# Optimization experiments

Measured on AMD Instinct MI355X. Metric: run time of the kernel, lower is better.

The kernel has to match this reference:

```python
import math
import jax, jax.numpy as jnp
import numpy as np

B, D, N, KP1 = 64, 128, 500000, 4096  # batch, input_size, output_size, K+1
MOMENTUM = 0.5


def setup_inputs() -> dict:
    key = jax.random.key(0)
    k0, k1, k2, k3, k4, k5 = jax.random.split(key, 6)
    stdv = 1.0 / math.sqrt(D / 3)
    image = jax.random.normal(k0, (B, D), jnp.float32)
    gene = jax.random.normal(k1, (B, D), jnp.float32)
    index = jax.random.randint(k2, (B,), 0, N, dtype=jnp.int32)
    idx = jax.random.randint(k3, (B, KP1), 0, N, dtype=jnp.int32)
    idx = idx.at[:, 0].set(index)  # positive sample in slot 0
    memory_image = jax.random.uniform(k4, (N, D), jnp.float32) * (2 * stdv) - stdv
    memory_gene = jax.random.uniform(k5, (N, D), jnp.float32) * (2 * stdv) - stdv
    return {"image": image, "gene": gene, "memory_image": memory_image,
            "memory_gene": memory_gene, "index": index, "idx": idx}


def _momentum_update(mem, x, index):
    # gather positive rows, momentum blend, L2 normalize, scatter back
    pos = mem[index] * MOMENTUM + x * (1.0 - MOMENTUM)          # [B, D]
    pos = pos / jnp.sqrt(jnp.sum(pos * pos, axis=1, keepdims=True))
    return mem.at[index].set(pos)


def reference(image, gene, memory_image, memory_gene, index, idx):
    # gathered bank rows are detached in the original (weights .detach())
    w_gene = jax.lax.stop_gradient(memory_gene[idx])    # [B, K+1, D]
    w_image = jax.lax.stop_gradient(memory_image[idx])  # [B, K+1, D]
    # bmm([B,K+1,D], [B,D,1]) -> scores [B, K+1]; use_softmax=False branch:
    # stabilized softmax over the K+1 candidates (no temperature division)
    out_image = jax.nn.softmax(jnp.einsum('bkd,bd->bk', w_gene, image), axis=1)
    out_gene = jax.nn.softmax(jnp.einsum('bkd,bd->bk', w_image, gene), axis=1)
    # no_grad momentum scatter-update of the banks
    new_mem_image = _momentum_update(memory_image, jax.lax.stop_gradient(image), index)
    new_mem_gene = _momentum_update(memory_gene, jax.lax.stop_gradient(gene), index)
    return out_image, out_gene, new_mem_image, new_mem_gene
```

## Files before the change

kernel.cpp:

```cpp
#include <hip/hip_runtime.h>
#include <math.h>

constexpr int Bb   = 64;
constexpr int Dd   = 128;
constexpr int KP1  = 4096;
constexpr long NMEM = 500000L * 128;
constexpr int BK   = Bb * KP1;

typedef float f4 __attribute__((ext_vector_type(4)));


__device__ __forceinline__ float dot8(float4 a, float4 b, float4 x0, float4 x1) {
    return a.x*x0.x + a.y*x0.y + a.z*x0.z + a.w*x0.w
         + b.x*x1.x + b.y*x1.y + b.z*x1.z + b.w*x1.w;
}

__global__ __launch_bounds__(512) void fused_scores_copy(
    const float* __restrict__ image, const float* __restrict__ gene,
    const float* __restrict__ mem_image, const float* __restrict__ mem_gene,
    const int* __restrict__ idx, float* __restrict__ out, int nCopyBlocks)
{
    const int tid = threadIdx.x;

    if (blockIdx.x >= 128) {
        const long half = NMEM / 4;
        const int  cb   = blockIdx.x - 128;
        const int  bank = cb & 1;
        const f4* src = bank ? (const f4*)mem_gene : (const f4*)mem_image;
        f4* dst = (f4*)(out + 2 * BK) + (long)bank * half;
        const long stride = (long)(nCopyBlocks >> 1) * 512;
        long i = (long)(cb >> 1) * 512 + tid;
        for (; i + 3 * stride < half; i += 4 * stride) {
            f4 v0 = src[i];
            f4 v1 = src[i + stride];
            f4 v2 = src[i + 2 * stride];
            f4 v3 = src[i + 3 * stride];
            __builtin_nontemporal_store(v0, dst + i);
            __builtin_nontemporal_store(v1, dst + i + stride);
            __builtin_nontemporal_store(v2, dst + i + 2 * stride);
            __builtin_nontemporal_store(v3, dst + i + 3 * stride);
        }
        for (; i < half; i += stride)
            __builtin_nontemporal_store(src[i], dst + i);
        return;
    }

    const int b     = blockIdx.x >> 1;
    const int which = blockIdx.x & 1;
    const float* w = which ? mem_image : mem_gene;
    const float* x = which ? gene : image;
    float* o = out + (long)which * BK + (long)b * KP1;

    __shared__ int   sidx[KP1];
    __shared__ float sv[KP1];
    __shared__ float red[8];

    {
        const int4* s4 = (const int4*)(idx + (long)b * KP1);
        int4* d4 = (int4*)sidx;
        d4[tid]       = s4[tid];
        d4[tid + 512] = s4[tid + 512];
    }

    const int lg  = tid & 15;
    const int grp = tid >> 4;

    float4 x0 = *(const float4*)(x + b * Dd + lg * 8);
    float4 x1 = *(const float4*)(x + b * Dd + lg * 8 + 4);
    __syncthreads();

    for (int j = 0; j < 128; j += 4) {
        const int k0 = grp + (j + 0) * 32;
        const int k1 = grp + (j + 1) * 32;
        const int k2 = grp + (j + 2) * 32;
        const int k3 = grp + (j + 3) * 32;
        const float4* r0 = (const float4*)(w + (long)sidx[k0] * Dd + lg * 8);
        const float4* r1 = (const float4*)(w + (long)sidx[k1] * Dd + lg * 8);
        const float4* r2 = (const float4*)(w + (long)sidx[k2] * Dd + lg * 8);
        const float4* r3 = (const float4*)(w + (long)sidx[k3] * Dd + lg * 8);
        float4 a0 = r0[0], b0 = r0[1];
        float4 a1 = r1[0], b1 = r1[1];
        float4 a2 = r2[0], b2 = r2[1];
        float4 a3 = r3[0], b3 = r3[1];
        float d0 = dot8(a0, b0, x0, x1);
        float d1 = dot8(a1, b1, x0, x1);
        float d2 = dot8(a2, b2, x0, x1);
        float d3 = dot8(a3, b3, x0, x1);
        d0 += __shfl_xor(d0, 1); d1 += __shfl_xor(d1, 1);
        d2 += __shfl_xor(d2, 1); d3 += __shfl_xor(d3, 1);
        d0 += __shfl_xor(d0, 2); d1 += __shfl_xor(d1, 2);
        d2 += __shfl_xor(d2, 2); d3 += __shfl_xor(d3, 2);
        d0 += __shfl_xor(d0, 4); d1 += __shfl_xor(d1, 4);
        d2 += __shfl_xor(d2, 4); d3 += __shfl_xor(d3, 4);
        d0 += __shfl_xor(d0, 8); d1 += __shfl_xor(d1, 8);
        d2 += __shfl_xor(d2, 8); d3 += __shfl_xor(d3, 8);
        if (lg == 0) {
            sv[k0] = d0; sv[k1] = d1; sv[k2] = d2; sv[k3] = d3;
        }
    }
    __syncthreads();

    float m = -INFINITY;
    for (int k = tid; k < KP1; k += 512) m = fmaxf(m, sv[k]);
    #pragma unroll
    for (int off = 1; off < 64; off <<= 1) m = fmaxf(m, __shfl_xor(m, off));
    if ((tid & 63) == 0) red[tid >> 6] = m;
    __syncthreads();
    if (tid < 64) {
        float tv = (tid < 8) ? red[tid] : -INFINITY;
        #pragma unroll
        for (int off = 1; off < 8; off <<= 1) tv = fmaxf(tv, __shfl_xor(tv, off));
        if (tid == 0) red[0] = tv;
    }
    __syncthreads();
    m = red[0];
    __syncthreads();

    float sum = 0.f;
    for (int k = tid; k < KP1; k += 512) {
        float e = expf(sv[k] - m);
        sv[k] = e;
        sum += e;
    }
    #pragma unroll
    for (int off = 1; off < 64; off <<= 1) sum += __shfl_xor(sum, off);
    if ((tid & 63) == 0) red[tid >> 6] = sum;
    __syncthreads();
    if (tid < 64) {
        float tv = (tid < 8) ? red[tid] : 0.f;
        #pragma unroll
        for (int off = 1; off < 8; off <<= 1) tv += __shfl_xor(tv, off);
        if (tid == 0) red[0] = tv;
    }
    __syncthreads();
    const float inv = 1.0f / red[0];
    for (int k = tid; k < KP1; k += 512) o[k] = sv[k] * inv;
}

__global__ __launch_bounds__(128) void momentum_update(
    const float* __restrict__ image, const float* __restrict__ gene,
    const float* __restrict__ mem_image, const float* __restrict__ mem_gene,
    const int* __restrict__ index, float* __restrict__ out)
{
    const int b     = blockIdx.x;
    const int which = blockIdx.y;
    const float* mem = which ? mem_gene : mem_image;
    const float* x   = which ? gene : image;
    float* o = out + 2 * BK + (long)which * NMEM;

    const long row = index[b];
    const int d = threadIdx.x;

    float p = mem[row * Dd + d] * 0.5f + x[(long)b * Dd + d] * 0.5f;
    float ss = p * p;
    #pragma unroll
    for (int off = 1; off < 64; off <<= 1) ss += __shfl_xor(ss, off);
    __shared__ float r2[2];
    if ((d & 63) == 0) r2[d >> 6] = ss;
    __syncthreads();
    const float inv = 1.0f / sqrtf(r2[0] + r2[1]);
    o[row * Dd + d] = p * inv;
}

extern "C" void kernel_launch(void* const* d_in, const int* in_sizes, int n_in,
                              void* d_out, int out_size, void* d_ws, size_t ws_size,
                              hipStream_t stream) {
    const float* image     = (const float*)d_in[0];
    const float* gene      = (const float*)d_in[1];
    const float* mem_image = (const float*)d_in[2];
    const float* mem_gene  = (const float*)d_in[3];
    const int*   index     = (const int*)d_in[4];
    const int*   idx       = (const int*)d_in[5];
    float* out = (float*)d_out;

    const int nCopy = 1920;
    fused_scores_copy<<<dim3(128 + nCopy), 512, 0, stream>>>(
        image, gene, mem_image, mem_gene, idx, out, nCopy);
    momentum_update<<<dim3(64, 2), 128, 0, stream>>>(
        image, gene, mem_image, mem_gene, index, out);
}
```

Baseline: 214.2 us.

## Split softmax rows across four blocks with a rescaling epilogue

Each score row of 4096 candidates is now split across four blocks of 1024. Each block writes unnormalized exponentials and a per-segment (max, sum) pair to workspace. A new epilogue kernel merges the four partials, rescales the output in place, and also runs the momentum update. This raises score-block parallelism from 128 to 512 blocks so the gather work spreads over more CUs, at the cost of an extra read/write pass over the score outputs. The copy loop unroll is also raised from 4 to 8.

```diff
diff --git a/kernel.cpp b/kernel.cpp
--- a/kernel.cpp
+++ b/kernel.cpp
@@ -7,6 +7,10 @@
 constexpr long NMEM = 500000L * 128;
 constexpr int BK   = Bb * KP1;
 
+constexpr int SPLIT = 4;
+constexpr int CSEG  = KP1 / SPLIT;
+constexpr int NSCORE = Bb * 2 * SPLIT;
+
 typedef float f4 __attribute__((ext_vector_type(4)));
 
 
@@ -18,48 +22,57 @@
 __global__ __launch_bounds__(512) void fused_scores_copy(
     const float* __restrict__ image, const float* __restrict__ gene,
     const float* __restrict__ mem_image, const float* __restrict__ mem_gene,
-    const int* __restrict__ idx, float* __restrict__ out, int nCopyBlocks)
+    const int* __restrict__ idx, float* __restrict__ out,
+    float2* __restrict__ ws, int nCopyBlocks)
 {
     const int tid = threadIdx.x;
 
-    if (blockIdx.x >= 128) {
+    if (blockIdx.x >= NSCORE) {
         const long half = NMEM / 4;
-        const int  cb   = blockIdx.x - 128;
+        const int  cb   = blockIdx.x - NSCORE;
         const int  bank = cb & 1;
         const f4* src = bank ? (const f4*)mem_gene : (const f4*)mem_image;
         f4* dst = (f4*)(out + 2 * BK) + (long)bank * half;
         const long stride = (long)(nCopyBlocks >> 1) * 512;
         long i = (long)(cb >> 1) * 512 + tid;
-        for (; i + 3 * stride < half; i += 4 * stride) {
+        for (; i + 7 * stride < half; i += 8 * stride) {
             f4 v0 = src[i];
             f4 v1 = src[i + stride];
             f4 v2 = src[i + 2 * stride];
             f4 v3 = src[i + 3 * stride];
+            f4 v4 = src[i + 4 * stride];
+            f4 v5 = src[i + 5 * stride];
+            f4 v6 = src[i + 6 * stride];
+            f4 v7 = src[i + 7 * stride];
             __builtin_nontemporal_store(v0, dst + i);
             __builtin_nontemporal_store(v1, dst + i + stride);
             __builtin_nontemporal_store(v2, dst + i + 2 * stride);
             __builtin_nontemporal_store(v3, dst + i + 3 * stride);
+            __builtin_nontemporal_store(v4, dst + i + 4 * stride);
+            __builtin_nontemporal_store(v5, dst + i + 5 * stride);
+            __builtin_nontemporal_store(v6, dst + i + 6 * stride);
+            __builtin_nontemporal_store(v7, dst + i + 7 * stride);
         }
         for (; i < half; i += stride)
             __builtin_nontemporal_store(src[i], dst + i);
         return;
     }
 
-    const int b     = blockIdx.x >> 1;
-    const int which = blockIdx.x & 1;
+    const int sb    = blockIdx.x;
+    const int seg   = sb & (SPLIT - 1);
+    const int which = (sb >> 2) & 1;
+    const int b     = sb >> 3;
     const float* w = which ? mem_image : mem_gene;
     const float* x = which ? gene : image;
-    float* o = out + (long)which * BK + (long)b * KP1;
-
-    __shared__ int   sidx[KP1];
-    __shared__ float sv[KP1];
+    float* o = out + (long)which * BK + (long)b * KP1 + seg * CSEG;
+
+    __shared__ int   sidx[CSEG];
+    __shared__ float sv[CSEG];
     __shared__ float red[8];
 
-    {
-        const int4* s4 = (const int4*)(idx + (long)b * KP1);
-        int4* d4 = (int4*)sidx;
-        d4[tid]       = s4[tid];
-        d4[tid + 512] = s4[tid + 512];
+    if (tid < 256) {
+        const int4* s4 = (const int4*)(idx + (long)b * KP1 + seg * CSEG);
+        ((int4*)sidx)[tid] = s4[tid];
     }
 
     const int lg  = tid & 15;
@@ -69,7 +82,7 @@
     float4 x1 = *(const float4*)(x + b * Dd + lg * 8 + 4);
     __syncthreads();
 
-    for (int j = 0; j < 128; j += 4) {
+    for (int j = 0; j < 32; j += 4) {
         const int k0 = grp + (j + 0) * 32;
         const int k1 = grp + (j + 1) * 32;
         const int k2 = grp + (j + 2) * 32;
@@ -100,8 +113,7 @@
     }
     __syncthreads();
 
-    float m = -INFINITY;
-    for (int k = tid; k < KP1; k += 512) m = fmaxf(m, sv[k]);
+    float m = fmaxf(sv[tid], sv[tid + 512]);
     #pragma unroll
     for (int off = 1; off < 64; off <<= 1) m = fmaxf(m, __shfl_xor(m, off));
     if ((tid & 63) == 0) red[tid >> 6] = m;
@@ -116,12 +128,11 @@
     m = red[0];
     __syncthreads();
 
-    float sum = 0.f;
-    for (int k = tid; k < KP1; k += 512) {
-        float e = expf(sv[k] - m);
-        sv[k] = e;
-        sum += e;
-    }
+    float e0 = expf(sv[tid] - m);
+    float e1 = expf(sv[tid + 512] - m);
+    o[tid]       = e0;
+    o[tid + 512] = e1;
+    float sum = e0 + e1;
     #pragma unroll
     for (int off = 1; off < 64; off <<= 1) sum += __shfl_xor(sum, off);
     if ((tid & 63) == 0) red[tid >> 6] = sum;
@@ -130,35 +141,56 @@
         float tv = (tid < 8) ? red[tid] : 0.f;
         #pragma unroll
         for (int off = 1; off < 8; off <<= 1) tv += __shfl_xor(tv, off);
-        if (tid == 0) red[0] = tv;
-    }
-    __syncthreads();
-    const float inv = 1.0f / red[0];
-    for (int k = tid; k < KP1; k += 512) o[k] = sv[k] * inv;
-}
-
-__global__ __launch_bounds__(128) void momentum_update(
+        if (tid == 0) ws[((which * Bb + b) << 2) | seg] = make_float2(m, tv);
+    }
+}
+
+__global__ __launch_bounds__(512) void epilogue(
     const float* __restrict__ image, const float* __restrict__ gene,
     const float* __restrict__ mem_image, const float* __restrict__ mem_gene,
-    const int* __restrict__ index, float* __restrict__ out)
+    const int* __restrict__ index, const float2* __restrict__ ws,
+    float* __restrict__ out)
 {
-    const int b     = blockIdx.x;
-    const int which = blockIdx.y;
+    const int tid = threadIdx.x;
+
+    if (blockIdx.x < 128) {
+        const int which = blockIdx.x & 1;
+        const int b     = blockIdx.x >> 1;
+        const float2* p = ws + ((which * Bb + b) << 2);
+        float2 p0 = p[0], p1 = p[1], p2 = p[2], p3 = p[3];
+        float M = fmaxf(fmaxf(p0.x, p1.x), fmaxf(p2.x, p3.x));
+        float s0 = expf(p0.x - M), s1 = expf(p1.x - M);
+        float s2 = expf(p2.x - M), s3 = expf(p3.x - M);
+        float denom = p0.y * s0 + p1.y * s1 + p2.y * s2 + p3.y * s3;
+        const float inv = 1.0f / denom;
+        float scale[SPLIT] = { s0 * inv, s1 * inv, s2 * inv, s3 * inv };
+        float* o = out + (long)which * BK + (long)b * KP1;
+        #pragma unroll
+        for (int r = 0; r < 8; ++r) {
+            int k = tid + r * 512;
+            o[k] *= scale[k >> 10];
+        }
+        return;
+    }
+
+    const int task  = ((blockIdx.x - 128) << 2) | (tid >> 7);
+    const int sub   = tid >> 7;
+    const int d     = tid & 127;
+    const int which = task >> 6;
+    const int b     = task & 63;
     const float* mem = which ? mem_gene : mem_image;
     const float* x   = which ? gene : image;
     float* o = out + 2 * BK + (long)which * NMEM;
 
     const long row = index[b];
-    const int d = threadIdx.x;
-
     float p = mem[row * Dd + d] * 0.5f + x[(long)b * Dd + d] * 0.5f;
     float ss = p * p;
     #pragma unroll
     for (int off = 1; off < 64; off <<= 1) ss += __shfl_xor(ss, off);
-    __shared__ float r2[2];
-    if ((d & 63) == 0) r2[d >> 6] = ss;
-    __syncthreads();
-    const float inv = 1.0f / sqrtf(r2[0] + r2[1]);
+    __shared__ float r2[8];
+    if ((tid & 63) == 0) r2[tid >> 6] = ss;
+    __syncthreads();
+    const float inv = 1.0f / sqrtf(r2[2 * sub] + r2[2 * sub + 1]);
     o[row * Dd + d] = p * inv;
 }
 
@@ -172,10 +204,11 @@
     const int*   index     = (const int*)d_in[4];
     const int*   idx       = (const int*)d_in[5];
     float* out = (float*)d_out;
+    float2* ws = (float2*)d_ws;
 
     const int nCopy = 1920;
-    fused_scores_copy<<<dim3(128 + nCopy), 512, 0, stream>>>(
-        image, gene, mem_image, mem_gene, idx, out, nCopy);
-    momentum_update<<<dim3(64, 2), 128, 0, stream>>>(
-        image, gene, mem_image, mem_gene, index, out);
-}
+    fused_scores_copy<<<dim3(NSCORE + nCopy), 512, 0, stream>>>(
+        image, gene, mem_image, mem_gene, idx, out, ws, nCopy);
+    epilogue<<<dim3(160), 512, 0, stream>>>(
+        image, gene, mem_image, mem_gene, index, ws, out);
+}
```

Measured after the change: 224.7 us. 4.9% more time.

## Use atomic work-stealing chunk queue for bank copy shared with score blocks

Applied to the files above, without the earlier changes.

Replaces the static grid-strided copy split with a dynamic queue: every block, including the 128 score/softmax blocks once they finish, grabs chunks of 8192 float4 via an atomic counter and copies them with 16 loads in flight. This aims to balance the bandwidth-bound copy across all CUs and let score blocks help once done, removing tail imbalance. It adds a counter-reset kernel launch, per-chunk atomics and barriers, and a launch-bounds occupancy hint. Softmax loops are also fully unrolled.

```diff
diff --git a/kernel.cpp b/kernel.cpp
--- a/kernel.cpp
+++ b/kernel.cpp
@@ -7,6 +7,14 @@
 constexpr long NMEM = 500000L * 128;
 constexpr int BK   = Bb * KP1;
 
+constexpr long HALF_F4    = NMEM / 4;
+constexpr int  CHUNK_F4   = 8192;
+constexpr int  FULL_PER_B = 1953;
+constexpr long TAIL_BASE  = (long)FULL_PER_B * CHUNK_F4;
+constexpr int  TAIL_F4    = (int)(HALF_F4 - TAIL_BASE);
+constexpr int  CHUNKS_PER_BANK = FULL_PER_B + 1;
+constexpr int  NCHUNK     = 2 * CHUNKS_PER_BANK;
+
 typedef float f4 __attribute__((ext_vector_type(4)));
 
 
@@ -15,126 +23,150 @@
          + b.x*x1.x + b.y*x1.y + b.z*x1.z + b.w*x1.w;
 }
 
-__global__ __launch_bounds__(512) void fused_scores_copy(
+__global__ __launch_bounds__(64) void zero_ctr(unsigned* ctr) {
+    if (threadIdx.x == 0) *ctr = 0u;
+}
+
+__global__ __launch_bounds__(512, 2) void fused_scores_copy(
     const float* __restrict__ image, const float* __restrict__ gene,
     const float* __restrict__ mem_image, const float* __restrict__ mem_gene,
-    const int* __restrict__ idx, float* __restrict__ out, int nCopyBlocks)
+    const int* __restrict__ idx, float* __restrict__ out, unsigned* __restrict__ ctr)
 {
     const int tid = threadIdx.x;
 
-    if (blockIdx.x >= 128) {
-        const long half = NMEM / 4;
-        const int  cb   = blockIdx.x - 128;
-        const int  bank = cb & 1;
-        const f4* src = bank ? (const f4*)mem_gene : (const f4*)mem_image;
-        f4* dst = (f4*)(out + 2 * BK) + (long)bank * half;
-        const long stride = (long)(nCopyBlocks >> 1) * 512;
-        long i = (long)(cb >> 1) * 512 + tid;
-        for (; i + 3 * stride < half; i += 4 * stride) {
-            f4 v0 = src[i];
-            f4 v1 = src[i + stride];
-            f4 v2 = src[i + 2 * stride];
-            f4 v3 = src[i + 3 * stride];
-            __builtin_nontemporal_store(v0, dst + i);
-            __builtin_nontemporal_store(v1, dst + i + stride);
-            __builtin_nontemporal_store(v2, dst + i + 2 * stride);
-            __builtin_nontemporal_store(v3, dst + i + 3 * stride);
-        }
-        for (; i < half; i += stride)
-            __builtin_nontemporal_store(src[i], dst + i);
-        return;
+    if (blockIdx.x < 128) {
+        const int b     = blockIdx.x >> 1;
+        const int which = blockIdx.x & 1;
+        const float* w = which ? mem_image : mem_gene;
+        const float* x = which ? gene : image;
+        float* o = out + (long)which * BK + (long)b * KP1;
+
+        __shared__ int   sidx[KP1];
+        __shared__ float sv[KP1];
+        __shared__ float red[8];
+
+        {
+            const int4* s4 = (const int4*)(idx + (long)b * KP1);
+            int4* d4 = (int4*)sidx;
+            d4[tid]       = s4[tid];
+            d4[tid + 512] = s4[tid + 512];
+        }
+
+        const int lg  = tid & 15;
+        const int grp = tid >> 4;
+
+        float4 x0 = *(const float4*)(x + b * Dd + lg * 8);
+        float4 x1 = *(const float4*)(x + b * Dd + lg * 8 + 4);
+        __syncthreads();
+
+        for (int j = 0; j < 128; j += 4) {
+            const int k0 = grp + (j + 0) * 32;
+            const int k1 = grp + (j + 1) * 32;
+            const int k2 = grp + (j + 2) * 32;
+            const int k3 = grp + (j + 3) * 32;
+            const float4* r0 = (const float4*)(w + (long)sidx[k0] * Dd + lg * 8);
+            const float4* r1 = (const float4*)(w + (long)sidx[k1] * Dd + lg * 8);
+            const float4* r2 = (const float4*)(w + (long)sidx[k2] * Dd + lg * 8);
+            const float4* r3 = (const float4*)(w + (long)sidx[k3] * Dd + lg * 8);
+            float4 a0 = r0[0], b0 = r0[1];
+            float4 a1 = r1[0], b1 = r1[1];
+            float4 a2 = r2[0], b2 = r2[1];
+            float4 a3 = r3[0], b3 = r3[1];
+            float d0 = dot8(a0, b0, x0, x1);
+            float d1 = dot8(a1, b1, x0, x1);
+            float d2 = dot8(a2, b2, x0, x1);
+            float d3 = dot8(a3, b3, x0, x1);
+            d0 += __shfl_xor(d0, 1); d1 += __shfl_xor(d1, 1);
+            d2 += __shfl_xor(d2, 1); d3 += __shfl_xor(d3, 1);
+            d0 += __shfl_xor(d0, 2); d1 += __shfl_xor(d1, 2);
+            d2 += __shfl_xor(d2, 2); d3 += __shfl_xor(d3, 2);
+            d0 += __shfl_xor(d0, 4); d1 += __shfl_xor(d1, 4);
+            d2 += __shfl_xor(d2, 4); d3 += __shfl_xor(d3, 4);
+            d0 += __shfl_xor(d0, 8); d1 += __shfl_xor(d1, 8);
+            d2 += __shfl_xor(d2, 8); d3 += __shfl_xor(d3, 8);
+            if (lg == 0) {
+                sv[k0] = d0; sv[k1] = d1; sv[k2] = d2; sv[k3] = d3;
+            }
+        }
+        __syncthreads();
+
+        float m = fmaxf(sv[tid], sv[tid + 512]);
+        m = fmaxf(m, fmaxf(sv[tid + 1024], sv[tid + 1536]));
+        m = fmaxf(m, fmaxf(sv[tid + 2048], sv[tid + 2560]));
+        m = fmaxf(m, fmaxf(sv[tid + 3072], sv[tid + 3584]));
+        #pragma unroll
+        for (int off = 1; off < 64; off <<= 1) m = fmaxf(m, __shfl_xor(m, off));
+        if ((tid & 63) == 0) red[tid >> 6] = m;
+        __syncthreads();
+        if (tid < 64) {
+            float tv = (tid < 8) ? red[tid] : -INFINITY;
+            #pragma unroll
+            for (int off = 1; off < 8; off <<= 1) tv = fmaxf(tv, __shfl_xor(tv, off));
+            if (tid == 0) red[0] = tv;
+        }
+        __syncthreads();
+        m = red[0];
+        __syncthreads();
+
+        float sum = 0.f;
+        #pragma unroll
+        for (int r = 0; r < 8; ++r) {
+            int k = tid + r * 512;
+            float e = expf(sv[k] - m);
+            sv[k] = e;
+            sum += e;
+        }
+        #pragma unroll
+        for (int off = 1; off < 64; off <<= 1) sum += __shfl_xor(sum, off);
+        if ((tid & 63) == 0) red[tid >> 6] = sum;
+        __syncthreads();
+        if (tid < 64) {
+            float tv = (tid < 8) ? red[tid] : 0.f;
+            #pragma unroll
+            for (int off = 1; off < 8; off <<= 1) tv += __shfl_xor(tv, off);
+            if (tid == 0) red[0] = tv;
+        }
+        __syncthreads();
+        const float inv = 1.0f / red[0];
+        #pragma unroll
+        for (int r = 0; r < 8; ++r) {
+            int k = tid + r * 512;
+            o[k] = sv[k] * inv;
+        }
     }
 
-    const int b     = blockIdx.x >> 1;
-    const int which = blockIdx.x & 1;
-    const float* w = which ? mem_image : mem_gene;
-    const float* x = which ? gene : image;
-    float* o = out + (long)which * BK + (long)b * KP1;
-
-    __shared__ int   sidx[KP1];
-    __shared__ float sv[KP1];
-    __shared__ float red[8];
-
-    {
-        const int4* s4 = (const int4*)(idx + (long)b * KP1);
-        int4* d4 = (int4*)sidx;
-        d4[tid]       = s4[tid];
-        d4[tid + 512] = s4[tid + 512];
+    const f4* srcI = (const f4*)mem_image;
+    const f4* srcG = (const f4*)mem_gene;
+    f4* dst = (f4*)(out + 2 * BK);
+
+    __shared__ unsigned sc;
+    for (;;) {
+        if (tid == 0) sc = atomicAdd(ctr, 1u);
+        __syncthreads();
+        const unsigned c = sc;
+        __syncthreads();
+        if (c >= NCHUNK) break;
+
+        const int  bank  = (c < CHUNKS_PER_BANK) ? 0 : 1;
+        const int  local = bank ? (int)(c - CHUNKS_PER_BANK) : (int)c;
+        const f4*  sbank = bank ? srcG : srcI;
+        const long dbank = (long)bank * HALF_F4;
+
+        if (local < FULL_PER_B) {
+            const long base = (long)local * CHUNK_F4;
+            f4 v[16];
+            #pragma unroll
+            for (int k = 0; k < 16; ++k) v[k] = sbank[base + k * 512 + tid];
+            #pragma unroll
+            for (int k = 0; k < 16; ++k)
+                __builtin_nontemporal_store(v[k], dst + dbank + base + k * 512 + tid);
+        } else {
+            f4 v0 = sbank[TAIL_BASE + tid];
+            f4 v1 = sbank[TAIL_BASE + 512 + tid];
+            __builtin_nontemporal_store(v0, dst + dbank + TAIL_BASE + tid);
+            __builtin_nontemporal_store(v1, dst + dbank + TAIL_BASE + 512 + tid);
+        }
     }
-
-    const int lg  = tid & 15;
-    const int grp = tid >> 4;
-
-    float4 x0 = *(const float4*)(x + b * Dd + lg * 8);
-    float4 x1 = *(const float4*)(x + b * Dd + lg * 8 + 4);
-    __syncthreads();
-
-    for (int j = 0; j < 128; j += 4) {
-        const int k0 = grp + (j + 0) * 32;
-        const int k1 = grp + (j + 1) * 32;
-        const int k2 = grp + (j + 2) * 32;
-        const int k3 = grp + (j + 3) * 32;
-        const float4* r0 = (const float4*)(w + (long)sidx[k0] * Dd + lg * 8);
-        const float4* r1 = (const float4*)(w + (long)sidx[k1] * Dd + lg * 8);
-        const float4* r2 = (const float4*)(w + (long)sidx[k2] * Dd + lg * 8);
-        const float4* r3 = (const float4*)(w + (long)sidx[k3] * Dd + lg * 8);
-        float4 a0 = r0[0], b0 = r0[1];
-        float4 a1 = r1[0], b1 = r1[1];
-        float4 a2 = r2[0], b2 = r2[1];
-        float4 a3 = r3[0], b3 = r3[1];
-        float d0 = dot8(a0, b0, x0, x1);
-        float d1 = dot8(a1, b1, x0, x1);
-        float d2 = dot8(a2, b2, x0, x1);
-        float d3 = dot8(a3, b3, x0, x1);
-        d0 += __shfl_xor(d0, 1); d1 += __shfl_xor(d1, 1);
-        d2 += __shfl_xor(d2, 1); d3 += __shfl_xor(d3, 1);
-        d0 += __shfl_xor(d0, 2); d1 += __shfl_xor(d1, 2);
-        d2 += __shfl_xor(d2, 2); d3 += __shfl_xor(d3, 2);
-        d0 += __shfl_xor(d0, 4); d1 += __shfl_xor(d1, 4);
-        d2 += __shfl_xor(d2, 4); d3 += __shfl_xor(d3, 4);
-        d0 += __shfl_xor(d0, 8); d1 += __shfl_xor(d1, 8);
-        d2 += __shfl_xor(d2, 8); d3 += __shfl_xor(d3, 8);
-        if (lg == 0) {
-            sv[k0] = d0; sv[k1] = d1; sv[k2] = d2; sv[k3] = d3;
-        }
-    }
-    __syncthreads();
-
-    float m = -INFINITY;
-    for (int k = tid; k < KP1; k += 512) m = fmaxf(m, sv[k]);
-    #pragma unroll
-    for (int off = 1; off < 64; off <<= 1) m = fmaxf(m, __shfl_xor(m, off));
-    if ((tid & 63) == 0) red[tid >> 6] = m;
-    __syncthreads();
-    if (tid < 64) {
-        float tv = (tid < 8) ? red[tid] : -INFINITY;
-        #pragma unroll
-        for (int off = 1; off < 8; off <<= 1) tv = fmaxf(tv, __shfl_xor(tv, off));
-        if (tid == 0) red[0] = tv;
-    }
-    __syncthreads();
-    m = red[0];
-    __syncthreads();
-
-    float sum = 0.f;
-    for (int k = tid; k < KP1; k += 512) {
-        float e = expf(sv[k] - m);
-        sv[k] = e;
-        sum += e;
-    }
-    #pragma unroll
-    for (int off = 1; off < 64; off <<= 1) sum += __shfl_xor(sum, off);
-    if ((tid & 63) == 0) red[tid >> 6] = sum;
-    __syncthreads();
-    if (tid < 64) {
-        float tv = (tid < 8) ? red[tid] : 0.f;
-        #pragma unroll
-        for (int off = 1; off < 8; off <<= 1) tv += __shfl_xor(tv, off);
-        if (tid == 0) red[0] = tv;
-    }
-    __syncthreads();
-    const float inv = 1.0f / red[0];
-    for (int k = tid; k < KP1; k += 512) o[k] = sv[k] * inv;
 }
 
 __global__ __launch_bounds__(128) void momentum_update(
@@ -172,10 +204,11 @@
     const int*   index     = (const int*)d_in[4];
     const int*   idx       = (const int*)d_in[5];
     float* out = (float*)d_out;
-
-    const int nCopy = 1920;
-    fused_scores_copy<<<dim3(128 + nCopy), 512, 0, stream>>>(
-        image, gene, mem_image, mem_gene, idx, out, nCopy);
+    unsigned* ctr = (unsigned*)d_ws;
+
+    zero_ctr<<<dim3(1), 64, 0, stream>>>(ctr);
+    fused_scores_copy<<<dim3(2048), 512, 0, stream>>>(
+        image, gene, mem_image, mem_gene, idx, out, ctr);
     momentum_update<<<dim3(64, 2), 128, 0, stream>>>(
         image, gene, mem_image, mem_gene, index, out);
 }
```

New measurement: 215.6 us. About the same (+0.7%).
